# Optimization experiments

Hardware: AMD Instinct MI355X
Metric: run time of the kernel (lower is better)

The kernel has to match this reference:

```python
import jax, jax.numpy as jnp
import numpy as np

N_NODES = 100000
N_EDGES = 1600000
T = 64          # num_timesteps (graphs)
D_IN = 256
D_H = 256
D_OUT = 16


def setup_inputs() -> dict:
    key = jax.random.key(0)
    ks = jax.random.split(key, 10)
    s = 1.0 / np.sqrt(D_H)
    x = jax.random.normal(ks[0], (N_NODES, D_IN), dtype=jnp.float32)
    edge_index = jax.random.randint(ks[1], (2, N_EDGES), 0, N_NODES, dtype=jnp.int64)
    ptr = (jnp.arange(T + 1, dtype=jnp.int64) * (N_NODES // T))  # even split of nodes into T snapshots
    return {
        "x": x,
        "edge_index": edge_index,
        "ptr": ptr,
        "W1": jax.random.normal(ks[2], (D_IN, D_H), dtype=jnp.float32) * s,
        "b1": jnp.zeros((D_H,), dtype=jnp.float32),
        "W2": jax.random.normal(ks[3], (D_H, D_H), dtype=jnp.float32) * s,
        "b2": jnp.zeros((D_H,), dtype=jnp.float32),
        "w_ih": jax.random.normal(ks[4], (3 * D_H, D_H), dtype=jnp.float32) * s,
        "w_hh": jax.random.normal(ks[5], (3 * D_H, D_H), dtype=jnp.float32) * s,
        "b_ih": jnp.zeros((3 * D_H,), dtype=jnp.float32),
        "b_hh": jnp.zeros((3 * D_H,), dtype=jnp.float32),
        "Wc": jax.random.normal(ks[6], (D_OUT, D_H), dtype=jnp.float32) * s,
        "bc": jnp.zeros((D_OUT,), dtype=jnp.float32),
    }


def _gcn_conv(x, W, b, src, dst, deg_inv_sqrt):
    # PyG GCNConv with self-loops: out_i = sum_j 1/sqrt(d_i d_j) * (x_j W) + (1/d_i) x_i W + b
    xw = x @ W                                            # [N, H]
    coef = deg_inv_sqrt[src] * deg_inv_sqrt[dst]          # [E]
    msg = xw[src] * coef[:, None]                         # [E, H] gather-scale
    agg = jax.ops.segment_sum(msg, dst, num_segments=N_NODES)
    return agg + xw * (deg_inv_sqrt ** 2)[:, None] + b


def _gru_final(seq, w_ih, w_hh, b_ih, b_hh):
    # torch nn.GRU, 1 layer, gate order (r, z, n). seq: [T, H] (batch=1)
    def step(h, x):
        gx = x @ w_ih.T + b_ih
        gh = h @ w_hh.T + b_hh
        xr, xz, xn = jnp.split(gx, 3)
        hr, hz, hn = jnp.split(gh, 3)
        r = jax.nn.sigmoid(xr + hr)
        z = jax.nn.sigmoid(xz + hz)
        n = jnp.tanh(xn + r * hn)
        h_new = (1.0 - z) * n + z * h
        return h_new, None
    h0 = jnp.zeros((D_H,), dtype=seq.dtype)
    h_final, _ = jax.lax.scan(step, h0, seq)
    return h_final


def reference(x, edge_index, ptr, W1, b1, W2, b2, w_ih, w_hh, b_ih, b_hh, Wc, bc):
    src, dst = edge_index[0], edge_index[1]
    # degree with self-loops
    deg = jax.ops.segment_sum(jnp.ones_like(dst, dtype=x.dtype), dst, num_segments=N_NODES) + 1.0
    deg_inv_sqrt = jax.lax.rsqrt(deg)

    h = jax.nn.relu(_gcn_conv(x, W1, b1, src, dst, deg_inv_sqrt))
    h = jax.nn.relu(_gcn_conv(h, W2, b2, src, dst, deg_inv_sqrt))

    # global_mean_pool over timestep segments derived from ptr
    seg = jnp.searchsorted(ptr, jnp.arange(N_NODES), side="right") - 1      # [N]
    sums = jax.ops.segment_sum(h, seg, num_segments=T)                       # [T, H]
    counts = (ptr[1:] - ptr[:-1]).astype(h.dtype)                            # [T]
    h_pooled = sums / jnp.maximum(counts, 1.0)[:, None]

    h_final = _gru_final(h_pooled, w_ih, w_hh, b_ih, b_hh)                   # [H]
    out = h_final @ Wc.T + bc                                                # [D_OUT]
    return out[None, :]                                                     # [1, D_OUT]
```

## Files before the change

kernel.cpp:

```cpp
#include <hip/hip_runtime.h>
#include <hip/hip_bf16.h>
#include <math.h>


static inline size_t align512(size_t x){ return (x + 511) & ~size_t(511); }

typedef _Float16 h2_t __attribute__((ext_vector_type(2)));
typedef unsigned short ushort_t;
typedef short bf16x8 __attribute__((ext_vector_type(8)));
typedef float f32x4 __attribute__((ext_vector_type(4)));
typedef float f32x2 __attribute__((ext_vector_type(2)));

#if defined(__has_builtin)
#if __has_builtin(__builtin_amdgcn_fdot2)
#define HAS_FDOT2 1
#endif
#if __has_builtin(__builtin_amdgcn_cvt_pk_f32_fp8) && __has_builtin(__builtin_amdgcn_cvt_pk_fp8_f32)
#define HAS_FP8CVT 1
#endif
#endif

__device__ inline ushort_t f2bf(float f){
  unsigned u = __float_as_uint(f);
  unsigned r = u + 0x7FFFu + ((u >> 16) & 1u);
  return (ushort_t)(r >> 16);
}
__device__ inline float bf2f(ushort_t h){ return __uint_as_float(((unsigned)h) << 16); }
__device__ inline unsigned pk2bf(float lo, float hi){
  return ((unsigned)f2bf(hi) << 16) | (unsigned)f2bf(lo);
}
__device__ inline bf16x8 as_bf16x8(uint4 u){
  union { uint4 u4; bf16x8 b; } c; c.u4 = u; return c.b;
}


__device__ inline unsigned char f2fp8(float x){
#ifdef HAS_FP8CVT
  int p = __builtin_amdgcn_cvt_pk_fp8_f32(x, x, 0, false);
  return (unsigned char)(p & 0xFF);
#else
  unsigned u = __float_as_uint(x);
  unsigned s = (u >> 24) & 0x80u;
  unsigned um = u & 0x7FFFFFFFu;
  if (um >= 0x43E00000u) return (unsigned char)(s | 0x7E);
  if (um <  0x3C000000u) return (unsigned char)s;
  unsigned r = um + 0x7FFFFu + ((um >> 20) & 1u);
  unsigned e = (r >> 23) & 0xFF, m = (r >> 20) & 7u;
  return (unsigned char)(s | ((e - 120u) << 3) | m);
#endif
}
__device__ inline void fp8x4_to_f32(unsigned v, float& a, float& b, float& c, float& d){
#ifdef HAS_FP8CVT
  f32x2 lo = __builtin_amdgcn_cvt_pk_f32_fp8(v, false);
  f32x2 hi = __builtin_amdgcn_cvt_pk_f32_fp8(v, true);
  a = lo.x; b = lo.y; c = hi.x; d = hi.y;
#else
  auto d1 = [](unsigned char t)->float{
    unsigned s = (t >> 7) & 1u, e = (t >> 3) & 0xFu, m = t & 7u;
    float v = (e == 0) ? ldexpf((float)m, -9) : ldexpf(8.0f + (float)m, (int)e - 10);
    return s ? -v : v;
  };
  a = d1(v & 0xFF); b = d1((v >> 8) & 0xFF); c = d1((v >> 16) & 0xFF); d = d1(v >> 24);
#endif
}


__global__ void count_kernel(const int* __restrict__ ei, int* __restrict__ cnt, int E){
  int e = blockIdx.x*256 + threadIdx.x;
  if (e < E) atomicAdd(&cnt[ei[E + e]], 1);
}

__global__ void dis_kernel(const int* __restrict__ cnt, float* __restrict__ dis, int N){
  int i = blockIdx.x*256 + threadIdx.x;
  if (i < N) dis[i] = rsqrtf((float)cnt[i] + 1.0f);
}

__global__ void scan_block_kernel(const int* __restrict__ cnt, int* __restrict__ rp,
                                  int* __restrict__ bsum, int N){
  __shared__ int s[2][1024];
  int t = threadIdx.x; int i = blockIdx.x*1024 + t;
  int v = (i < N) ? cnt[i] : 0;
  int cur = 0; s[0][t] = v; __syncthreads();
  for (int off = 1; off < 1024; off <<= 1){
    int nxt = cur ^ 1;
    int val = s[cur][t];
    if (t >= off) val += s[cur][t - off];
    s[nxt][t] = val; cur = nxt; __syncthreads();
  }
  if (i < N) rp[i+1] = s[cur][t];
  if (t == 1023) bsum[blockIdx.x] = s[cur][1023];
}

__global__ void scan_sums_kernel(int* __restrict__ bsum, int nb){
  __shared__ int s[128];
  int t = threadIdx.x;
  if (t < nb) s[t] = bsum[t];
  __syncthreads();
  if (t == 0){ int acc = 0; for (int b = 0; b < nb; b++){ int v = s[b]; s[b] = acc; acc += v; } }
  __syncthreads();
  if (t < nb) bsum[t] = s[t];
}

__global__ void add_off_kernel(int* __restrict__ rp, const int* __restrict__ bsum,
                               int* __restrict__ cnt, int N){
  int i = blockIdx.x*256 + threadIdx.x;
  if (i < N){ rp[i+1] += bsum[i >> 10]; cnt[i] = 0; }
  if (i == 0) rp[0] = 0;
}

__global__ void fill_kernel(const int* __restrict__ ei, const int* __restrict__ rp,
                            int* __restrict__ cnt, int* __restrict__ csrc, int E){
  int e = blockIdx.x*256 + threadIdx.x;
  if (e < E){
    int s = ei[e]; int d = ei[E + e];
    int pos = rp[d] + atomicAdd(&cnt[d], 1);
    csrc[pos] = s;
  }
}


__global__ void packW_kernel(const float* __restrict__ W, uint4* __restrict__ Wp){
  int idx = blockIdx.x*256 + threadIdx.x;
  int lane = idx & 63;
  int blk  = idx >> 6;
  int q    = blk & 7;
  int t16  = blk >> 3;
  int n = t16*16 + (lane & 15);
  int k = q*32 + (lane >> 4)*8;
  uint4 v;
  v.x = pk2bf(W[(size_t)(k+0)*256 + n], W[(size_t)(k+1)*256 + n]);
  v.y = pk2bf(W[(size_t)(k+2)*256 + n], W[(size_t)(k+3)*256 + n]);
  v.z = pk2bf(W[(size_t)(k+4)*256 + n], W[(size_t)(k+5)*256 + n]);
  v.w = pk2bf(W[(size_t)(k+6)*256 + n], W[(size_t)(k+7)*256 + n]);
  Wp[idx] = v;
}


template<bool A_BF16>
__global__ __launch_bounds__(256, 2) void gemm_mfma(const void* __restrict__ Ap,
                                                    const uint4* __restrict__ Wp,
                                                    unsigned char* __restrict__ out, int N){
  __shared__ __align__(16) ushort_t As[2][128][40];
  int tid  = threadIdx.x;
  int lane = tid & 63;
  int wave = tid >> 6;
  int wr = wave >> 1, wc = wave & 1;
  int quad = lane >> 4;
  int l15  = lane & 15;
  int r0 = blockIdx.x * 128;
  int cb = blockIdx.y;

  uint4 bfr[4][8];
  {
    const uint4* wpb = Wp + (size_t)(cb*2 + wc) * 2048;
    #pragma unroll
    for (int ct = 0; ct < 4; ct++)
      #pragma unroll
      for (int q = 0; q < 8; q++)
        bfr[ct][q] = wpb[(ct*8 + q)*64 + lane];
  }

  f32x4 acc[4][4];
  #pragma unroll
  for (int rt = 0; rt < 4; rt++)
    #pragma unroll
    for (int ct = 0; ct < 4; ct++)
      acc[rt][ct] = f32x4{0.f, 0.f, 0.f, 0.f};

  int srow = tid >> 1;
  int shalf = tid & 1;
  int grow = min(r0 + srow, N - 1);

  auto load_stage = [&](int it, uint4& v0, uint4& v1){
    int k0 = it*32 + shalf*16;
    if constexpr (A_BF16){
      const ushort_t* Ab = (const ushort_t*)Ap;
      const uint4* ga = (const uint4*)(Ab + (size_t)grow*256 + k0);
      v0 = ga[0]; v1 = ga[1];
    } else {
      const float* Af = (const float*)Ap;
      const float4* ga = (const float4*)(Af + (size_t)grow*256 + k0);
      float4 f0 = ga[0], f1 = ga[1], f2 = ga[2], f3 = ga[3];
      v0.x = pk2bf(f0.x, f0.y); v0.y = pk2bf(f0.z, f0.w);
      v0.z = pk2bf(f1.x, f1.y); v0.w = pk2bf(f1.z, f1.w);
      v1.x = pk2bf(f2.x, f2.y); v1.y = pk2bf(f2.z, f2.w);
      v1.z = pk2bf(f3.x, f3.y); v1.w = pk2bf(f3.z, f3.w);
    }
  };
  auto write_stage = [&](int b, uint4 v0, uint4 v1){
    *(uint4*)&As[b][srow][shalf*16]     = v0;
    *(uint4*)&As[b][srow][shalf*16 + 8] = v1;
  };

  {
    uint4 v0, v1;
    load_stage(0, v0, v1);
    write_stage(0, v0, v1);
  }
  __syncthreads();

  #pragma unroll
  for (int it = 0; it < 8; it++){
    const int b = it & 1;
    uint4 n0, n1;
    if (it < 7) load_stage(it + 1, n0, n1);
    #pragma unroll
    for (int rt = 0; rt < 4; rt++){
      int arow = wr*64 + rt*16 + l15;
      uint4 av = *(const uint4*)&As[b][arow][quad*8];
      bf16x8 af = as_bf16x8(av);
      #pragma unroll
      for (int ct = 0; ct < 4; ct++)
        acc[rt][ct] = __builtin_amdgcn_mfma_f32_16x16x32_bf16(
            af, as_bf16x8(bfr[ct][it]), acc[rt][ct], 0, 0, 0);
    }
    if (it < 7){
      write_stage(b ^ 1, n0, n1);
      __syncthreads();
    }
  }

  int crow0 = r0 + wr*64 + quad*4;
  int ccol0 = cb*128 + wc*64 + l15;
  #pragma unroll
  for (int rt = 0; rt < 4; rt++){
    #pragma unroll
    for (int g = 0; g < 4; g++){
      int row = crow0 + rt*16 + g;
      if (row < N){
        #pragma unroll
        for (int ct = 0; ct < 4; ct++)
          out[(size_t)row*256 + ccol0 + ct*16] = f2fp8(acc[rt][ct][g]);
      }
    }
  }
}


__global__ __launch_bounds__(256) void agg_kernel(const unsigned char* __restrict__ xw,
                                                  const float* __restrict__ dis,
                                                  const int* __restrict__ rp,
                                                  const int* __restrict__ csrc,
                                                  const float* __restrict__ bias,
                                                  ushort_t* __restrict__ out, int N){
  int node = blockIdx.x*8 + (threadIdx.x >> 5);
  int lane = threadIdx.x & 31;
  if (node >= N) return;
  const uint2* xw2 = (const uint2*)xw;
  float di = dis[node];
  float sc = di * di;
  float acc[8];
  {
    uint2 a = xw2[(size_t)node*32 + lane];
    float v0,v1,v2,v3,v4,v5,v6,v7;
    fp8x4_to_f32(a.x, v0, v1, v2, v3);
    fp8x4_to_f32(a.y, v4, v5, v6, v7);
    acc[0]=v0*sc; acc[1]=v1*sc; acc[2]=v2*sc; acc[3]=v3*sc;
    acc[4]=v4*sc; acc[5]=v5*sc; acc[6]=v6*sc; acc[7]=v7*sc;
  }
  int e0 = rp[node], e1 = rp[node+1];
  for (int e = e0; e < e1; e++){
    int s = csrc[e];
    float cc = dis[s] * di;
    uint2 v = xw2[(size_t)s*32 + lane];
    float v0,v1,v2,v3,v4,v5,v6,v7;
    fp8x4_to_f32(v.x, v0, v1, v2, v3);
    fp8x4_to_f32(v.y, v4, v5, v6, v7);
    acc[0] = fmaf(v0, cc, acc[0]);
    acc[1] = fmaf(v1, cc, acc[1]);
    acc[2] = fmaf(v2, cc, acc[2]);
    acc[3] = fmaf(v3, cc, acc[3]);
    acc[4] = fmaf(v4, cc, acc[4]);
    acc[5] = fmaf(v5, cc, acc[5]);
    acc[6] = fmaf(v6, cc, acc[6]);
    acc[7] = fmaf(v7, cc, acc[7]);
  }
  const float4* b4 = (const float4*)bias;
  float4 bA = b4[lane*2], bB = b4[lane*2+1];
  acc[0] = fmaxf(acc[0] + bA.x, 0.f);
  acc[1] = fmaxf(acc[1] + bA.y, 0.f);
  acc[2] = fmaxf(acc[2] + bA.z, 0.f);
  acc[3] = fmaxf(acc[3] + bA.w, 0.f);
  acc[4] = fmaxf(acc[4] + bB.x, 0.f);
  acc[5] = fmaxf(acc[5] + bB.y, 0.f);
  acc[6] = fmaxf(acc[6] + bB.z, 0.f);
  acc[7] = fmaxf(acc[7] + bB.w, 0.f);
  uint4 o;
  o.x = pk2bf(acc[0], acc[1]);
  o.y = pk2bf(acc[2], acc[3]);
  o.z = pk2bf(acc[4], acc[5]);
  o.w = pk2bf(acc[6], acc[7]);
  ((uint4*)out)[(size_t)node*32 + lane] = o;
}


__global__ void pool_kernel(const ushort_t* __restrict__ h, const int* __restrict__ ptr,
                            float* __restrict__ hp){
  int t = blockIdx.x; int part = blockIdx.y; int c = threadIdx.x;
  int s0 = ptr[t], s1 = ptr[t+1];
  int len = s1 - s0;
  int chunk = (len + 7) / 8;
  int r0 = s0 + part*chunk;
  int r1 = min(r0 + chunk, s1);
  float acc = 0.f;
  for (int r = r0; r < r1; r++) acc += bf2f(h[(size_t)r*256 + c]);
  if (r1 > r0) atomicAdd(&hp[t*256 + c], acc);
}

__global__ void hp_div_kernel(float* __restrict__ hp, const int* __restrict__ ptr){
  int t = blockIdx.x; int c = threadIdx.x;
  float cf = (float)max(ptr[t+1] - ptr[t], 1);
  hp[t*256 + c] /= cf;
}


__global__ __launch_bounds__(768) void gx_kernel(const float* __restrict__ hp,
                                                 const float* __restrict__ wih,
                                                 const float* __restrict__ bih,
                                                 float* __restrict__ gx){
  __shared__ float xs[256];
  int t = blockIdx.x; int g = threadIdx.x;
  if (g < 256) xs[g] = hp[t*256 + g];
  __syncthreads();
  float acc = bih[g];
  const float* wr = wih + (size_t)g*256;
  #pragma unroll 4
  for (int k = 0; k < 256; k++) acc = fmaf(xs[k], wr[k], acc);
  gx[t*768 + g] = acc;
}


__global__ __launch_bounds__(512, 2) void gru_kernel(const float* __restrict__ gx,
                                                     const float* __restrict__ whh,
                                                     const float* __restrict__ bhh,
                                                     const float* __restrict__ Wc,
                                                     const float* __restrict__ bc,
                                                     float* __restrict__ out){
  __shared__ _Float16 hh[256];
  __shared__ float hfin[256];
  int tid = threadIdx.x;
  int i = tid >> 1;
  int half = tid & 1;

  h2_t wr[64], wz[64], wn[64];
  {
    const float2* w2 = (const float2*)whh;
    size_t base = (size_t)half * 64;
    const float2* pr = w2 + (size_t)i*128       + base;
    const float2* pz = w2 + (size_t)(i+256)*128 + base;
    const float2* pn = w2 + (size_t)(i+512)*128 + base;
    #pragma unroll
    for (int k = 0; k < 64; k++){
      float2 a = pr[k];
      float2 b = pz[k];
      float2 c = pn[k];
      wr[k] = h2_t{(_Float16)a.x, (_Float16)a.y};
      wz[k] = h2_t{(_Float16)b.x, (_Float16)b.y};
      wn[k] = h2_t{(_Float16)c.x, (_Float16)c.y};
    }
  }
  float bR = bhh[i], bZ = bhh[i+256], bN = bhh[i+512];
  float h = 0.f;

  for (int t = 0; t < 64; t++){
    if (half == 0) hh[i] = (_Float16)h;
    __syncthreads();
    float gxr = gx[t*768 + i];
    float gxz = gx[t*768 + 256 + i];
    float gxn = gx[t*768 + 512 + i];
    const h2_t* hp2 = ((const h2_t*)hh) + half*64;
    float accR = 0.f, accZ = 0.f, accN = 0.f;
    #pragma unroll
    for (int k = 0; k < 64; k++){
      h2_t hv = hp2[k];
#ifdef HAS_FDOT2
      accR = __builtin_amdgcn_fdot2(hv, wr[k], accR, false);
      accZ = __builtin_amdgcn_fdot2(hv, wz[k], accZ, false);
      accN = __builtin_amdgcn_fdot2(hv, wn[k], accN, false);
#else
      accR = fmaf((float)hv.x, (float)wr[k].x, accR);
      accR = fmaf((float)hv.y, (float)wr[k].y, accR);
      accZ = fmaf((float)hv.x, (float)wz[k].x, accZ);
      accZ = fmaf((float)hv.y, (float)wz[k].y, accZ);
      accN = fmaf((float)hv.x, (float)wn[k].x, accN);
      accN = fmaf((float)hv.y, (float)wn[k].y, accN);
#endif
    }
    accR += __shfl_xor(accR, 1);
    accZ += __shfl_xor(accZ, 1);
    accN += __shfl_xor(accN, 1);
    float r = 1.f/(1.f + expf(-(gxr + accR + bR)));
    float z = 1.f/(1.f + expf(-(gxz + accZ + bZ)));
    float n = tanhf(gxn + r*(accN + bN));
    float hnew = (1.f - z)*n + z*h;
    __syncthreads();
    h = hnew;
  }

  if (half == 0) hfin[i] = h;
  __syncthreads();
  if (tid < 16){
    float acc = bc[tid];
    const float* wrow = Wc + (size_t)tid*256;
    for (int k = 0; k < 256; k++) acc = fmaf(hfin[k], wrow[k], acc);
    out[tid] = acc;
  }
}

extern "C" void kernel_launch(void* const* d_in, const int* in_sizes, int n_in,
                              void* d_out, int out_size, void* d_ws, size_t ws_size,
                              hipStream_t stream){
  const float* x   = (const float*)d_in[0];
  const int*   ei  = (const int*)d_in[1];
  const int*   ptr = (const int*)d_in[2];
  const float* W1  = (const float*)d_in[3];
  const float* b1  = (const float*)d_in[4];
  const float* W2  = (const float*)d_in[5];
  const float* b2  = (const float*)d_in[6];
  const float* wih = (const float*)d_in[7];
  const float* whh = (const float*)d_in[8];
  const float* bih = (const float*)d_in[9];
  const float* bhh = (const float*)d_in[10];
  const float* Wc  = (const float*)d_in[11];
  const float* bc  = (const float*)d_in[12];
  float* outp = (float*)d_out;

  const int N = in_sizes[0] / 256;
  const int E = in_sizes[1] / 2;

  char* w = (char*)d_ws;
  size_t off = 0;
  auto alloc = [&](size_t bytes){ void* p = w + off; off = align512(off + bytes); return p; };
  unsigned char* bufA = (unsigned char*)alloc((size_t)N*256);
  ushort_t*      bufB = (ushort_t*)alloc((size_t)N*256*2);
  float* dis  = (float*)alloc((size_t)N*4);
  int*   cnt  = (int*)  alloc((size_t)N*4);
  int*   rp   = (int*)  alloc((size_t)(N+1)*4);
  int*   bsum = (int*)  alloc(128*4);
  int*   csrc = (int*)  alloc((size_t)E*4);
  uint4* Wp1  = (uint4*)alloc(8192*16);
  uint4* Wp2  = (uint4*)alloc(8192*16);
  float* hp   = (float*)alloc((size_t)64*256*4);
  float* gxb  = (float*)alloc((size_t)64*768*4);
  (void)ws_size; (void)n_in; (void)out_size;

  hipMemsetAsync(cnt, 0, (size_t)N*4, stream);
  hipMemsetAsync(hp,  0, (size_t)64*256*4, stream);

  count_kernel<<<(E+255)/256, 256, 0, stream>>>(ei, cnt, E);
  dis_kernel<<<(N+255)/256, 256, 0, stream>>>(cnt, dis, N);
  int nb = (N + 1023) / 1024;
  scan_block_kernel<<<nb, 1024, 0, stream>>>(cnt, rp, bsum, N);
  scan_sums_kernel<<<1, 128, 0, stream>>>(bsum, nb);
  add_off_kernel<<<(N+255)/256, 256, 0, stream>>>(rp, bsum, cnt, N);
  fill_kernel<<<(E+255)/256, 256, 0, stream>>>(ei, rp, cnt, csrc, E);
  packW_kernel<<<32, 256, 0, stream>>>(W1, Wp1);
  packW_kernel<<<32, 256, 0, stream>>>(W2, Wp2);

  gemm_mfma<false><<<dim3((N+127)/128, 2), 256, 0, stream>>>(x, Wp1, bufA, N);
  agg_kernel<<<(N+7)/8, 256, 0, stream>>>(bufA, dis, rp, csrc, b1, bufB, N);
  gemm_mfma<true><<<dim3((N+127)/128, 2), 256, 0, stream>>>(bufB, Wp2, bufA, N);
  agg_kernel<<<(N+7)/8, 256, 0, stream>>>(bufA, dis, rp, csrc, b2, bufB, N);

  pool_kernel<<<dim3(64, 8), 256, 0, stream>>>(bufB, ptr, hp);
  hp_div_kernel<<<64, 256, 0, stream>>>(hp, ptr);
  gx_kernel<<<64, 768, 0, stream>>>(hp, wih, bih, gxb);
  gru_kernel<<<1, 512, 0, stream>>>(gxb, whh, bhh, Wc, bc, outp);
}
```

Measured before the change: 817.5 us.

## Restructure GRU kernel: 4-way split, double-buffered h, one barrier per step

Folds the mean-pool division into gx_kernel, which removes one launch. The serial GRU kernel now runs 1024 threads with a 4-way split of the dot product, so each thread handles 32 pairs and uses two accumulators per gate. A double-buffered shared h array means each timestep needs only one barrier, and the next step's gx values are prefetched. Sigmoid and tanh use fast exp/rcp approximations, trading slight precision for shorter latency on the critical path.

```diff
diff --git a/kernel.cpp b/kernel.cpp
--- a/kernel.cpp
+++ b/kernel.cpp
@@ -307,20 +307,18 @@
   if (r1 > r0) atomicAdd(&hp[t*256 + c], acc);
 }
 
-__global__ void hp_div_kernel(float* __restrict__ hp, const int* __restrict__ ptr){
-  int t = blockIdx.x; int c = threadIdx.x;
-  float cf = (float)max(ptr[t+1] - ptr[t], 1);
-  hp[t*256 + c] /= cf;
-}
-
 
 __global__ __launch_bounds__(768) void gx_kernel(const float* __restrict__ hp,
+                                                 const int* __restrict__ ptr,
                                                  const float* __restrict__ wih,
                                                  const float* __restrict__ bih,
                                                  float* __restrict__ gx){
   __shared__ float xs[256];
   int t = blockIdx.x; int g = threadIdx.x;
-  if (g < 256) xs[g] = hp[t*256 + g];
+  if (g < 256){
+    float cf = (float)max(ptr[t+1] - ptr[t], 1);
+    xs[g] = hp[t*256 + g] / cf;
+  }
   __syncthreads();
   float acc = bih[g];
   const float* wr = wih + (size_t)g*256;
@@ -330,80 +328,115 @@
 }
 
 
-__global__ __launch_bounds__(512, 2) void gru_kernel(const float* __restrict__ gx,
-                                                     const float* __restrict__ whh,
-                                                     const float* __restrict__ bhh,
-                                                     const float* __restrict__ Wc,
-                                                     const float* __restrict__ bc,
-                                                     float* __restrict__ out){
-  __shared__ _Float16 hh[256];
+__device__ inline float fast_sig(float x){
+  return __builtin_amdgcn_rcpf(1.f + __expf(-x));
+}
+__device__ inline float fast_tanh(float x){
+  return 1.f - 2.f*__builtin_amdgcn_rcpf(1.f + __expf(2.f*x));
+}
+
+__global__ __launch_bounds__(1024, 4) void gru_kernel(const float* __restrict__ gx,
+                                                      const float* __restrict__ whh,
+                                                      const float* __restrict__ bhh,
+                                                      const float* __restrict__ Wc,
+                                                      const float* __restrict__ bc,
+                                                      float* __restrict__ out){
+  __shared__ _Float16 hh[2][256];
   __shared__ float hfin[256];
   int tid = threadIdx.x;
-  int i = tid >> 1;
-  int half = tid & 1;
-
-  h2_t wr[64], wz[64], wn[64];
+  int i = tid >> 2;
+  int q = tid & 3;
+
+  h2_t wrg[32], wzg[32], wng[32];
   {
     const float2* w2 = (const float2*)whh;
-    size_t base = (size_t)half * 64;
+    size_t base = (size_t)q * 32;
     const float2* pr = w2 + (size_t)i*128       + base;
     const float2* pz = w2 + (size_t)(i+256)*128 + base;
     const float2* pn = w2 + (size_t)(i+512)*128 + base;
     #pragma unroll
-    for (int k = 0; k < 64; k++){
+    for (int k = 0; k < 32; k++){
       float2 a = pr[k];
       float2 b = pz[k];
       float2 c = pn[k];
-      wr[k] = h2_t{(_Float16)a.x, (_Float16)a.y};
-      wz[k] = h2_t{(_Float16)b.x, (_Float16)b.y};
-      wn[k] = h2_t{(_Float16)c.x, (_Float16)c.y};
+      wrg[k] = h2_t{(_Float16)a.x, (_Float16)a.y};
+      wzg[k] = h2_t{(_Float16)b.x, (_Float16)b.y};
+      wng[k] = h2_t{(_Float16)c.x, (_Float16)c.y};
     }
   }
   float bR = bhh[i], bZ = bhh[i+256], bN = bhh[i+512];
+  if (tid < 256) hh[0][tid] = (_Float16)0.f;
   float h = 0.f;
+  float gxr = gx[i], gxz = gx[256 + i], gxn = gx[512 + i];
+  __syncthreads();
 
   for (int t = 0; t < 64; t++){
-    if (half == 0) hh[i] = (_Float16)h;
+    float ngr = 0.f, ngz = 0.f, ngn = 0.f;
+    if (t < 63){
+      const float* g = gx + (size_t)(t+1)*768;
+      ngr = g[i]; ngz = g[256 + i]; ngn = g[512 + i];
+    }
+    const h2_t* hp2 = ((const h2_t*)hh[t & 1]) + q*32;
+    float aR0=0.f, aR1=0.f, aZ0=0.f, aZ1=0.f, aN0=0.f, aN1=0.f;
+    #pragma unroll
+    for (int k = 0; k < 32; k += 2){
+      h2_t h0 = hp2[k];
+      h2_t h1 = hp2[k+1];
+#ifdef HAS_FDOT2
+      aR0 = __builtin_amdgcn_fdot2(h0, wrg[k],   aR0, false);
+      aZ0 = __builtin_amdgcn_fdot2(h0, wzg[k],   aZ0, false);
+      aN0 = __builtin_amdgcn_fdot2(h0, wng[k],   aN0, false);
+      aR1 = __builtin_amdgcn_fdot2(h1, wrg[k+1], aR1, false);
+      aZ1 = __builtin_amdgcn_fdot2(h1, wzg[k+1], aZ1, false);
+      aN1 = __builtin_amdgcn_fdot2(h1, wng[k+1], aN1, false);
+#else
+      aR0 = fmaf((float)h0.x, (float)wrg[k].x, aR0);
+      aR0 = fmaf((float)h0.y, (float)wrg[k].y, aR0);
+      aZ0 = fmaf((float)h0.x, (float)wzg[k].x, aZ0);
+      aZ0 = fmaf((float)h0.y, (float)wzg[k].y, aZ0);
+      aN0 = fmaf((float)h0.x, (float)wng[k].x, aN0);
+      aN0 = fmaf((float)h0.y, (float)wng[k].y, aN0);
+      aR1 = fmaf((float)h1.x, (float)wrg[k+1].x, aR1);
+      aR1 = fmaf((float)h1.y, (float)wrg[k+1].y, aR1);
+      aZ1 = fmaf((float)h1.x, (float)wzg[k+1].x, aZ1);
+      aZ1 = fmaf((float)h1.y, (float)wzg[k+1].y, aZ1);
+      aN1 = fmaf((float)h1.x, (float)wng[k+1].x, aN1);
+      aN1 = fmaf((float)h1.y, (float)wng[k+1].y, aN1);
+#endif
+    }
+    float accR = aR0 + aR1, accZ = aZ0 + aZ1, accN = aN0 + aN1;
+    accR += __shfl_xor(accR, 1); accR += __shfl_xor(accR, 2);
+    accZ += __shfl_xor(accZ, 1); accZ += __shfl_xor(accZ, 2);
+    accN += __shfl_xor(accN, 1); accN += __shfl_xor(accN, 2);
+    float r = fast_sig(gxr + accR + bR);
+    float z = fast_sig(gxz + accZ + bZ);
+    float n = fast_tanh(gxn + r*(accN + bN));
+    float hnew = (1.f - z)*n + z*h;
+    if (q == 0) hh[(t & 1) ^ 1][i] = (_Float16)hnew;
+    gxr = ngr; gxz = ngz; gxn = ngn;
+    h = hnew;
     __syncthreads();
-    float gxr = gx[t*768 + i];
-    float gxz = gx[t*768 + 256 + i];
-    float gxn = gx[t*768 + 512 + i];
-    const h2_t* hp2 = ((const h2_t*)hh) + half*64;
-    float accR = 0.f, accZ = 0.f, accN = 0.f;
-    #pragma unroll
-    for (int k = 0; k < 64; k++){
-      h2_t hv = hp2[k];
-#ifdef HAS_FDOT2
-      accR = __builtin_amdgcn_fdot2(hv, wr[k], accR, false);
-      accZ = __builtin_amdgcn_fdot2(hv, wz[k], accZ, false);
-      accN = __builtin_amdgcn_fdot2(hv, wn[k], accN, false);
-#else
-      accR = fmaf((float)hv.x, (float)wr[k].x, accR);
-      accR = fmaf((float)hv.y, (float)wr[k].y, accR);
-      accZ = fmaf((float)hv.x, (float)wz[k].x, accZ);
-      accZ = fmaf((float)hv.y, (float)wz[k].y, accZ);
-      accN = fmaf((float)hv.x, (float)wn[k].x, accN);
-      accN = fmaf((float)hv.y, (float)wn[k].y, accN);
-#endif
-    }
-    accR += __shfl_xor(accR, 1);
-    accZ += __shfl_xor(accZ, 1);
-    accN += __shfl_xor(accN, 1);
-    float r = 1.f/(1.f + expf(-(gxr + accR + bR)));
-    float z = 1.f/(1.f + expf(-(gxz + accZ + bZ)));
-    float n = tanhf(gxn + r*(accN + bN));
-    float hnew = (1.f - z)*n + z*h;
-    __syncthreads();
-    h = hnew;
-  }
-
-  if (half == 0) hfin[i] = h;
+  }
+
+  if (q == 0) hfin[i] = h;
   __syncthreads();
-  if (tid < 16){
-    float acc = bc[tid];
-    const float* wrow = Wc + (size_t)tid*256;
-    for (int k = 0; k < 256; k++) acc = fmaf(hfin[k], wrow[k], acc);
-    out[tid] = acc;
+  if (tid < 64){
+    int r = tid >> 2, qq = tid & 3;
+    const float4* wrow = (const float4*)(Wc + (size_t)r*256 + (size_t)qq*64);
+    const float4* hv = (const float4*)(hfin + (size_t)qq*64);
+    float acc = 0.f;
+    #pragma unroll
+    for (int k = 0; k < 16; k++){
+      float4 wv = wrow[k];
+      float4 xv = hv[k];
+      acc = fmaf(wv.x, xv.x, acc);
+      acc = fmaf(wv.y, xv.y, acc);
+      acc = fmaf(wv.z, xv.z, acc);
+      acc = fmaf(wv.w, xv.w, acc);
+    }
+    acc += __shfl_xor(acc, 1);
+    acc += __shfl_xor(acc, 2);
+    if (qq == 0) out[r] = acc + bc[r];
   }
 }
 
@@ -463,7 +496,6 @@
   agg_kernel<<<(N+7)/8, 256, 0, stream>>>(bufA, dis, rp, csrc, b2, bufB, N);
 
   pool_kernel<<<dim3(64, 8), 256, 0, stream>>>(bufB, ptr, hp);
-  hp_div_kernel<<<64, 256, 0, stream>>>(hp, ptr);
-  gx_kernel<<<64, 768, 0, stream>>>(hp, wih, bih, gxb);
-  gru_kernel<<<1, 512, 0, stream>>>(gxb, whh, bhh, Wc, bc, outp);
-}
+  gx_kernel<<<64, 768, 0, stream>>>(hp, ptr, wih, bih, gxb);
+  gru_kernel<<<1, 1024, 0, stream>>>(gxb, whh, bhh, Wc, bc, outp);
+}
```

After: 838.9 us. +2.6%, slower.
